# Optimization experiments

Hardware: AMD Instinct MI355X
Metric: run time of the kernel (lower is better)

Reference implementation:

```python
import jax, jax.numpy as jnp
import numpy as np

B, D_IN, UNITS = 4096, 1024, 1024


def setup_inputs() -> dict:
    key = jax.random.key(0)
    ks = jax.random.split(key, 8)
    scale = 1.0 / np.sqrt(D_IN + UNITS)
    return {
        "inputs": jax.random.normal(ks[0], (B, D_IN), jnp.float32),
        "hidden_state": jax.random.normal(ks[1], (B, UNITS), jnp.float32),
        "cell_state": jax.random.normal(ks[2], (B, UNITS), jnp.float32),
        "W_f": jax.random.normal(ks[3], (D_IN + UNITS, UNITS), jnp.float32) * scale,
        "b_f": jnp.ones((UNITS,), jnp.float32),  # forget gate bias initialized to ones
        "W_i": jax.random.normal(ks[4], (D_IN + UNITS, UNITS), jnp.float32) * scale,
        "b_i": jnp.zeros((UNITS,), jnp.float32),
        "W_c": jax.random.normal(ks[5], (D_IN + UNITS, UNITS), jnp.float32) * scale,
        "b_c": jnp.zeros((UNITS,), jnp.float32),
        "W_o": jax.random.normal(ks[6], (D_IN + UNITS, UNITS), jnp.float32) * scale,
        "b_o": jnp.zeros((UNITS,), jnp.float32),
    }


def reference(inputs, hidden_state, cell_state, W_f, b_f, W_i, b_i, W_c, b_c, W_o, b_o):
    # concat (hidden, inputs) along feature axis -> [B, UNITS + D_IN]
    x = jnp.concatenate((hidden_state, inputs), axis=1)
    # fuse the 4 gate projections into one GEMM: [B, 4*UNITS]
    W = jnp.concatenate((W_f, W_i, W_c, W_o), axis=1)
    b = jnp.concatenate((b_f, b_i, b_c, b_o), axis=0)
    gates = x @ W + b
    f, i, c, o = jnp.split(gates, 4, axis=1)
    forget_gate = jax.nn.sigmoid(f)
    input_gate = jax.nn.sigmoid(i)
    state_candidates = jnp.tanh(c)
    output_gate = jax.nn.sigmoid(o)
    new_cell = forget_gate * cell_state + input_gate * state_candidates
    new_hidden = output_gate * jnp.tanh(new_cell)
    return (new_hidden, new_cell)
```

## Files before the change

### kernel.cpp

```cpp
#include <hip/hip_runtime.h>

#define MDIM 4096
#define KDIM 2048
#define UDIM 1024
#define CMOFF (MDIM * UDIM)
#define NK 64
#define THREADS 512

typedef __bf16 bfrag __attribute__((ext_vector_type(8)));
typedef float f32x16 __attribute__((ext_vector_type(16)));

#define GLDS(gsrc, ldst)                                                                  \
  __builtin_amdgcn_global_load_lds((const __attribute__((address_space(1))) void*)(gsrc), \
                                   (__attribute__((address_space(3))) void*)(ldst), 16, 0, 0)

__device__ __forceinline__ unsigned short f2bf(float x) {
  unsigned int u = __float_as_uint(x);
  unsigned int r = (u + 0x7fffu + ((u >> 16) & 1u)) >> 16;
  return (unsigned short)r;
}

__device__ __forceinline__ float fast_sigmoid(float x) { return 1.f / (1.f + __expf(-x)); }

__device__ __forceinline__ float fast_tanh(float x) {
  float ax = fabsf(x);
  float e = __expf(-2.f * ax);
  float r = (1.f - e) / (1.f + e);
  return copysignf(r, x);
}

__global__ void pack_x(const float* __restrict__ hidden, const float* __restrict__ inputs,
                       unsigned short* __restrict__ A) {
  int t = blockIdx.x * blockDim.x + threadIdx.x;
  int e = t * 4;
  int m = e >> 11;
  int c = e & 2047;
  const float* src = (c < 1024) ? (hidden + m * 1024 + c) : (inputs + m * 1024 + (c - 1024));
  float4 v = *(const float4*)src;
  ushort4 o;
  o.x = f2bf(v.x);
  o.y = f2bf(v.y);
  o.z = f2bf(v.z);
  o.w = f2bf(v.w);
  *(ushort4*)(A + e) = o;
}

__global__ void pack_w(const float* __restrict__ Wf, const float* __restrict__ Wi,
                       const float* __restrict__ Wc, const float* __restrict__ Wo,
                       unsigned short* __restrict__ Wt) {
  __shared__ float tile[32][33];
  const int k0 = blockIdx.x * 32;
  const int u0 = blockIdx.y * 32;
  const int g = blockIdx.z;
  const float* W = (g == 0) ? Wf : (g == 1) ? Wi : (g == 2) ? Wc : Wo;
  const int t = threadIdx.x;
  {
    int kk = t >> 3, uu = (t & 7) * 4;
    float4 v = *(const float4*)(W + (k0 + kk) * UDIM + u0 + uu);
    tile[kk][uu + 0] = v.x;
    tile[kk][uu + 1] = v.y;
    tile[kk][uu + 2] = v.z;
    tile[kk][uu + 3] = v.w;
  }
  __syncthreads();
  {
    int ur = t >> 3, k4 = (t & 7) * 4;
    ushort4 o;
    o.x = f2bf(tile[k4 + 0][ur]);
    o.y = f2bf(tile[k4 + 1][ur]);
    o.z = f2bf(tile[k4 + 2][ur]);
    o.w = f2bf(tile[k4 + 3][ur]);
    *(ushort4*)(Wt + (size_t)(g * UDIM + u0 + ur) * KDIM + k0 + k4) = o;
  }
}

__global__ __launch_bounds__(THREADS, 2) void lstm_gemm(
    const unsigned short* __restrict__ A, const unsigned short* __restrict__ Wt,
    const float* __restrict__ bf_, const float* __restrict__ bi_,
    const float* __restrict__ bc_, const float* __restrict__ bo_,
    const float* __restrict__ cell, float* __restrict__ out) {
  extern __shared__ __bf16 lds[];

  const int tid = threadIdx.x;
  const int lane = tid & 63;
  const int wid = tid >> 6;
  const int wr = wid >> 1;
  const int wc = wid & 1;
  const int cl = lane & 31;
  const int hb = lane >> 5;

  const int wg = blockIdx.x;
  const int swz = (wg & 7) * 32 + (wg >> 3);
  const int m0 = (swz >> 4) * 256;
  const int bn = swz & 15;

  const int G0 = tid, G1 = THREADS + tid;
  const int ar0 = G0 >> 2, ar1 = G1 >> 2;
  const unsigned short* aS0 =
      A + (size_t)(m0 + ar0) * KDIM + (((G0 & 3) ^ ((ar0 >> 1) & 3)) * 8);
  const unsigned short* aS1 =
      A + (size_t)(m0 + ar1) * KDIM + (((G1 & 3) ^ ((ar1 >> 1) & 3)) * 8);
  const int nr0 = G0 >> 2, nr1 = G1 >> 2;
  const int u_0 = bn * 64 + ((nr0 >> 7) << 5) + (nr0 & 31);
  const int u_1 = bn * 64 + ((nr1 >> 7) << 5) + (nr1 & 31);
  const int g_0 = (nr0 >> 5) & 3;
  const int g_1 = (nr1 >> 5) & 3;
  const unsigned short* bS0 =
      Wt + (size_t)(g_0 * UDIM + u_0) * KDIM + (((G0 & 3) ^ ((nr0 >> 1) & 3)) * 8);
  const unsigned short* bS1 =
      Wt + (size_t)(g_1 * UDIM + u_1) * KDIM + (((G1 & 3) ^ ((nr1 >> 1) & 3)) * 8);

  int aoff2[2][2];
#pragma unroll
  for (int mf = 0; mf < 2; ++mf)
#pragma unroll
    for (int kk = 0; kk < 2; ++kk) {
      const int R = wr * 64 + mf * 32 + cl;
      aoff2[mf][kk] = R * 32 + (((kk * 2 + hb) ^ ((R >> 1) & 3)) * 8);
    }
  int boff2[4][2];
#pragma unroll
  for (int nf = 0; nf < 4; ++nf)
#pragma unroll
    for (int kk = 0; kk < 2; ++kk) {
      const int n = wc * 128 + nf * 32 + cl;
      boff2[nf][kk] = 8192 + n * 32 + (((kk * 2 + hb) ^ ((n >> 1) & 3)) * 8);
    }

  f32x16 acc[2][4];
#pragma unroll
  for (int mf = 0; mf < 2; ++mf)
#pragma unroll
    for (int nf = 0; nf < 4; ++nf)
#pragma unroll
      for (int j = 0; j < 16; ++j) acc[mf][nf][j] = 0.f;

#define STAGE_A(T, SR)                        \
  do {                                        \
    __bf16* dst_ = lds + (SR) * 16384;        \
    GLDS(aS0 + (T) * 32, dst_ + G0 * 8);      \
    GLDS(aS1 + (T) * 32, dst_ + G1 * 8);      \
  } while (0)
#define STAGE_B(T, SR)                        \
  do {                                        \
    __bf16* dst_ = lds + (SR) * 16384 + 8192; \
    GLDS(bS0 + (T) * 32, dst_ + G0 * 8);      \
    GLDS(bS1 + (T) * 32, dst_ + G1 * 8);      \
  } while (0)

  STAGE_A(0, 0);
  STAGE_B(0, 0);
  STAGE_A(1, 1);
  STAGE_B(1, 1);
  STAGE_A(2, 2);
  STAGE_B(2, 2);
  asm volatile("s_waitcnt vmcnt(8)" ::: "memory");
  __builtin_amdgcn_s_barrier();

#define TILE_BODY(T, R, SR, DO_STAGE, WAITCODE)                                          \
  do {                                                                                   \
    __bf16* ldsr_ = lds + (R) * 16384;                                                   \
    bfrag Af[2][2], Bf[4][2];                                                            \
    _Pragma("unroll") for (int mf = 0; mf < 2; ++mf) Af[mf][0] =                         \
        *(const bfrag*)(ldsr_ + aoff2[mf][0]);                                           \
    _Pragma("unroll") for (int nf = 0; nf < 4; ++nf) Bf[nf][0] =                         \
        *(const bfrag*)(ldsr_ + boff2[nf][0]);                                           \
    _Pragma("unroll") for (int mf = 0; mf < 2; ++mf) Af[mf][1] =                         \
        *(const bfrag*)(ldsr_ + aoff2[mf][1]);                                           \
    _Pragma("unroll") for (int nf = 0; nf < 4; ++nf) Bf[nf][1] =                         \
        *(const bfrag*)(ldsr_ + boff2[nf][1]);                                           \
    if (DO_STAGE) {                                                                      \
      STAGE_A((T) + 3, SR);                                                              \
      STAGE_B((T) + 3, SR);                                                              \
    }                                                                                    \
    __builtin_amdgcn_s_barrier();                                                        \
    __builtin_amdgcn_s_setprio(1);                                                       \
    _Pragma("unroll") for (int kk = 0; kk < 2; ++kk)                                     \
        _Pragma("unroll") for (int mf = 0; mf < 2; ++mf)                                 \
            _Pragma("unroll") for (int nf = 0; nf < 4; ++nf) acc[mf][nf] =               \
                __builtin_amdgcn_mfma_f32_32x32x16_bf16(Af[mf][kk], Bf[nf][kk],          \
                                                        acc[mf][nf], 0, 0, 0);           \
    __builtin_amdgcn_s_setprio(0);                                                       \
    WAITCODE;                                                                            \
    __builtin_amdgcn_s_barrier();                                                        \
  } while (0)

#define VM8 asm volatile("s_waitcnt vmcnt(8)" ::: "memory")
#define VM4 asm volatile("s_waitcnt vmcnt(4)" ::: "memory")
#define VM0 asm volatile("s_waitcnt vmcnt(0)" ::: "memory")

  for (int t = 0; t < NK - 4; t += 4) {
    TILE_BODY(t + 0, 0, 3, 1, VM8);
    TILE_BODY(t + 1, 1, 0, 1, VM8);
    TILE_BODY(t + 2, 2, 1, 1, VM8);
    TILE_BODY(t + 3, 3, 2, 1, VM8);
  }
  TILE_BODY(NK - 4, 0, 3, 1, VM8);
  TILE_BODY(NK - 3, 1, 0, 0, VM4);
  TILE_BODY(NK - 2, 2, 0, 0, VM0);
  TILE_BODY(NK - 1, 3, 0, 0, );

  const int u = bn * 64 + wc * 32 + cl;
  const float fb = bf_[u], ib = bi_[u], cb = bc_[u], ob = bo_[u];
  const int rbase = m0 + wr * 64 + 4 * hb;
#pragma unroll
  for (int mf = 0; mf < 2; ++mf) {
#pragma unroll
    for (int r = 0; r < 16; ++r) {
      const int m = rbase + mf * 32 + (r & 3) + 8 * (r >> 2);
      float pf = acc[mf][0][r] + fb;
      float pi = acc[mf][1][r] + ib;
      float pc = acc[mf][2][r] + cb;
      float po = acc[mf][3][r] + ob;
      float fg = fast_sigmoid(pf);
      float ig = fast_sigmoid(pi);
      float cc = fast_tanh(pc);
      float og = fast_sigmoid(po);
      float cold = cell[(size_t)m * UDIM + u];
      float cnew = fg * cold + ig * cc;
      out[(size_t)m * UDIM + u] = og * fast_tanh(cnew);
      out[CMOFF + (size_t)m * UDIM + u] = cnew;
    }
  }
}

extern "C" void kernel_launch(void* const* d_in, const int* in_sizes, int n_in,
                              void* d_out, int out_size, void* d_ws, size_t ws_size,
                              hipStream_t stream) {
  const float* inputs = (const float*)d_in[0];
  const float* hidden = (const float*)d_in[1];
  const float* cell = (const float*)d_in[2];
  const float* Wf = (const float*)d_in[3];
  const float* bf = (const float*)d_in[4];
  const float* Wi = (const float*)d_in[5];
  const float* bi = (const float*)d_in[6];
  const float* Wc = (const float*)d_in[7];
  const float* bc = (const float*)d_in[8];
  const float* Wo = (const float*)d_in[9];
  const float* bo = (const float*)d_in[10];
  float* out = (float*)d_out;

  unsigned short* Abf = (unsigned short*)d_ws;
  unsigned short* Wt = Abf + (size_t)MDIM * KDIM;

  pack_x<<<(MDIM * KDIM / 4) / 256, 256, 0, stream>>>(hidden, inputs, Abf);
  pack_w<<<dim3(KDIM / 32, UDIM / 32, 4), 256, 0, stream>>>(Wf, Wi, Wc, Wo, Wt);
  lstm_gemm<<<dim3(256), dim3(THREADS), 131072, stream>>>(Abf, Wt, bf, bi, bc, bo, cell, out);
}
```

Baseline: 99.18 us.

## Pre-pack operands into tile-contiguous blocks and switch GEMM to double-buffered K=64 steps

The pack kernels now write A and the transposed weights in a tile-blocked layout, so each 256x64 (A) or 256x64 (B) K-slab is one contiguous 32 KB chunk. The GEMM loads each slab with fully contiguous global_load_lds transfers and reads MFMA fragments with simple strided offsets, with no XOR swizzle. The old 4-deep ring of K=32 tiles becomes a 2-deep ring of K=64 tiles with a full vmcnt(0) wait per step. The aim is cheaper address math, fewer barriers and more coalesced packing. The trade-off is shallower prefetch, and the unswizzled LDS reads may cause bank conflicts.

```diff
diff --git a/kernel.cpp b/kernel.cpp
--- a/kernel.cpp
+++ b/kernel.cpp
@@ -4,7 +4,6 @@
 #define KDIM 2048
 #define UDIM 1024
 #define CMOFF (MDIM * UDIM)
-#define NK 64
 #define THREADS 512
 
 typedef __bf16 bfrag __attribute__((ext_vector_type(8)));
@@ -29,53 +28,68 @@
   return copysignf(r, x);
 }
 
+
 __global__ void pack_x(const float* __restrict__ hidden, const float* __restrict__ inputs,
-                       unsigned short* __restrict__ A) {
-  int t = blockIdx.x * blockDim.x + threadIdx.x;
-  int e = t * 4;
-  int m = e >> 11;
-  int c = e & 2047;
-  const float* src = (c < 1024) ? (hidden + m * 1024 + c) : (inputs + m * 1024 + (c - 1024));
-  float4 v = *(const float4*)src;
-  ushort4 o;
-  o.x = f2bf(v.x);
-  o.y = f2bf(v.y);
-  o.z = f2bf(v.z);
-  o.w = f2bf(v.w);
-  *(ushort4*)(A + e) = o;
+                       unsigned short* __restrict__ Apk) {
+  __shared__ uint4 t4[2048];
+  const int P = blockIdx.x;
+  const int S = blockIdx.y;
+  const int tid = threadIdx.x;
+  const size_t m = (size_t)P * 256 + tid;
+  const float* src = (S < 16) ? (hidden + m * 1024 + S * 64) : (inputs + m * 1024 + (S - 16) * 64);
+  const float4* s4 = (const float4*)src;
+#pragma unroll
+  for (int j = 0; j < 8; ++j) {
+    float4 v0 = s4[2 * j], v1 = s4[2 * j + 1];
+    uint4 g;
+    g.x = (unsigned)f2bf(v0.x) | ((unsigned)f2bf(v0.y) << 16);
+    g.y = (unsigned)f2bf(v0.z) | ((unsigned)f2bf(v0.w) << 16);
+    g.z = (unsigned)f2bf(v1.x) | ((unsigned)f2bf(v1.y) << 16);
+    g.w = (unsigned)f2bf(v1.z) | ((unsigned)f2bf(v1.w) << 16);
+    t4[j * 256 + tid] = g;
+  }
+  __syncthreads();
+  uint4* dst = (uint4*)(Apk + ((size_t)P * 32 + S) * 16384);
+#pragma unroll
+  for (int c = 0; c < 8; ++c) dst[c * 256 + tid] = t4[c * 256 + tid];
 }
 
 __global__ void pack_w(const float* __restrict__ Wf, const float* __restrict__ Wi,
                        const float* __restrict__ Wc, const float* __restrict__ Wo,
-                       unsigned short* __restrict__ Wt) {
-  __shared__ float tile[32][33];
-  const int k0 = blockIdx.x * 32;
-  const int u0 = blockIdx.y * 32;
-  const int g = blockIdx.z;
-  const float* W = (g == 0) ? Wf : (g == 1) ? Wi : (g == 2) ? Wc : Wo;
-  const int t = threadIdx.x;
-  {
-    int kk = t >> 3, uu = (t & 7) * 4;
-    float4 v = *(const float4*)(W + (k0 + kk) * UDIM + u0 + uu);
-    tile[kk][uu + 0] = v.x;
-    tile[kk][uu + 1] = v.y;
-    tile[kk][uu + 2] = v.z;
-    tile[kk][uu + 3] = v.w;
+                       unsigned short* __restrict__ Bpk) {
+  __shared__ unsigned short t1[4][64][64];
+  const int bn = blockIdx.x;
+  const int S = blockIdx.y;
+  const int tid = threadIdx.x;
+  const int q = tid >> 6, kk = tid & 63;
+  const float* W = (q == 0) ? Wf : (q == 1) ? Wi : (q == 2) ? Wc : Wo;
+  const float* src = W + (size_t)(S * 64 + kk) * UDIM + bn * 64;
+#pragma unroll
+  for (int i = 0; i < 16; ++i) {
+    float4 v = ((const float4*)src)[i];
+    t1[q][kk][i * 4 + 0] = f2bf(v.x);
+    t1[q][kk][i * 4 + 1] = f2bf(v.y);
+    t1[q][kk][i * 4 + 2] = f2bf(v.z);
+    t1[q][kk][i * 4 + 3] = f2bf(v.w);
   }
   __syncthreads();
-  {
-    int ur = t >> 3, k4 = (t & 7) * 4;
-    ushort4 o;
-    o.x = f2bf(tile[k4 + 0][ur]);
-    o.y = f2bf(tile[k4 + 1][ur]);
-    o.z = f2bf(tile[k4 + 2][ur]);
-    o.w = f2bf(tile[k4 + 3][ur]);
-    *(ushort4*)(Wt + (size_t)(g * UDIM + u0 + ur) * KDIM + k0 + k4) = o;
+  const int qp = (tid >> 5) & 3;
+  const int ul = ((tid >> 7) << 5) + (tid & 31);
+  uint4* dst = (uint4*)(Bpk + ((size_t)bn * 32 + S) * 16384);
+#pragma unroll
+  for (int c = 0; c < 8; ++c) {
+    const unsigned short* p = &t1[qp][c * 8][ul];
+    uint4 g;
+    g.x = (unsigned)p[0] | ((unsigned)p[64] << 16);
+    g.y = (unsigned)p[128] | ((unsigned)p[192] << 16);
+    g.z = (unsigned)p[256] | ((unsigned)p[320] << 16);
+    g.w = (unsigned)p[384] | ((unsigned)p[448] << 16);
+    dst[c * 256 + tid] = g;
   }
 }
 
 __global__ __launch_bounds__(THREADS, 2) void lstm_gemm(
-    const unsigned short* __restrict__ A, const unsigned short* __restrict__ Wt,
+    const unsigned short* __restrict__ Apk, const unsigned short* __restrict__ Bpk,
     const float* __restrict__ bf_, const float* __restrict__ bi_,
     const float* __restrict__ bc_, const float* __restrict__ bo_,
     const float* __restrict__ cell, float* __restrict__ out) {
@@ -91,114 +105,70 @@
 
   const int wg = blockIdx.x;
   const int swz = (wg & 7) * 32 + (wg >> 3);
-  const int m0 = (swz >> 4) * 256;
+  const int P = swz >> 4;
+  const int m0 = P * 256;
   const int bn = swz & 15;
 
-  const int G0 = tid, G1 = THREADS + tid;
-  const int ar0 = G0 >> 2, ar1 = G1 >> 2;
-  const unsigned short* aS0 =
-      A + (size_t)(m0 + ar0) * KDIM + (((G0 & 3) ^ ((ar0 >> 1) & 3)) * 8);
-  const unsigned short* aS1 =
-      A + (size_t)(m0 + ar1) * KDIM + (((G1 & 3) ^ ((ar1 >> 1) & 3)) * 8);
-  const int nr0 = G0 >> 2, nr1 = G1 >> 2;
-  const int u_0 = bn * 64 + ((nr0 >> 7) << 5) + (nr0 & 31);
-  const int u_1 = bn * 64 + ((nr1 >> 7) << 5) + (nr1 & 31);
-  const int g_0 = (nr0 >> 5) & 3;
-  const int g_1 = (nr1 >> 5) & 3;
-  const unsigned short* bS0 =
-      Wt + (size_t)(g_0 * UDIM + u_0) * KDIM + (((G0 & 3) ^ ((nr0 >> 1) & 3)) * 8);
-  const unsigned short* bS1 =
-      Wt + (size_t)(g_1 * UDIM + u_1) * KDIM + (((G1 & 3) ^ ((nr1 >> 1) & 3)) * 8);
-
-  int aoff2[2][2];
+  const unsigned short* aP = Apk + (size_t)P * 524288 + (size_t)tid * 8;
+  const unsigned short* bP = Bpk + (size_t)bn * 524288 + (size_t)tid * 8;
+
+  f32x16 acc[2][4];
 #pragma unroll
   for (int mf = 0; mf < 2; ++mf)
 #pragma unroll
-    for (int kk = 0; kk < 2; ++kk) {
-      const int R = wr * 64 + mf * 32 + cl;
-      aoff2[mf][kk] = R * 32 + (((kk * 2 + hb) ^ ((R >> 1) & 3)) * 8);
-    }
-  int boff2[4][2];
-#pragma unroll
-  for (int nf = 0; nf < 4; ++nf)
-#pragma unroll
-    for (int kk = 0; kk < 2; ++kk) {
-      const int n = wc * 128 + nf * 32 + cl;
-      boff2[nf][kk] = 8192 + n * 32 + (((kk * 2 + hb) ^ ((n >> 1) & 3)) * 8);
-    }
-
-  f32x16 acc[2][4];
-#pragma unroll
-  for (int mf = 0; mf < 2; ++mf)
-#pragma unroll
     for (int nf = 0; nf < 4; ++nf)
 #pragma unroll
       for (int j = 0; j < 16; ++j) acc[mf][nf][j] = 0.f;
 
-#define STAGE_A(T, SR)                        \
-  do {                                        \
-    __bf16* dst_ = lds + (SR) * 16384;        \
-    GLDS(aS0 + (T) * 32, dst_ + G0 * 8);      \
-    GLDS(aS1 + (T) * 32, dst_ + G1 * 8);      \
+  const int aBase = hb * 2048 + (wr * 64 + cl) * 8;
+  const int bBase = 16384 + hb * 2048 + (wc * 128 + cl) * 8;
+
+#define STAGE(RING)                                                               \
+  do {                                                                            \
+    _Pragma("unroll") for (int c = 0; c < 4; ++c)                                 \
+        GLDS(aP + c * 4096, lds + (RING) * 32768 + c * 4096 + tid * 8);           \
+    _Pragma("unroll") for (int c = 0; c < 4; ++c)                                 \
+        GLDS(bP + c * 4096, lds + (RING) * 32768 + 16384 + c * 4096 + tid * 8);   \
+    aP += 16384;                                                                  \
+    bP += 16384;                                                                  \
   } while (0)
-#define STAGE_B(T, SR)                        \
-  do {                                        \
-    __bf16* dst_ = lds + (SR) * 16384 + 8192; \
-    GLDS(bS0 + (T) * 32, dst_ + G0 * 8);      \
-    GLDS(bS1 + (T) * 32, dst_ + G1 * 8);      \
+
+#define STEP_BODY(RING, DO_STAGE)                                                     \
+  do {                                                                                \
+    asm volatile("s_waitcnt vmcnt(0)" ::: "memory");                                  \
+    __builtin_amdgcn_s_barrier();                                                     \
+    __builtin_amdgcn_sched_barrier(0);                                                \
+    if (DO_STAGE) STAGE((RING) ^ 1);                                                  \
+    const __bf16* apl = lds + (RING) * 32768 + aBase;                                 \
+    const __bf16* bpl = lds + (RING) * 32768 + bBase;                                 \
+    _Pragma("unroll") for (int ks = 0; ks < 4; ++ks) {                                \
+      bfrag a0 = *(const bfrag*)(apl + ks * 4096);                                    \
+      bfrag a1 = *(const bfrag*)(apl + ks * 4096 + 256);                              \
+      bfrag b0 = *(const bfrag*)(bpl + ks * 4096);                                    \
+      bfrag b1 = *(const bfrag*)(bpl + ks * 4096 + 256);                              \
+      bfrag b2 = *(const bfrag*)(bpl + ks * 4096 + 512);                              \
+      bfrag b3 = *(const bfrag*)(bpl + ks * 4096 + 768);                              \
+      __builtin_amdgcn_s_setprio(1);                                                  \
+      acc[0][0] = __builtin_amdgcn_mfma_f32_32x32x16_bf16(a0, b0, acc[0][0], 0, 0, 0);\
+      acc[0][1] = __builtin_amdgcn_mfma_f32_32x32x16_bf16(a0, b1, acc[0][1], 0, 0, 0);\
+      acc[0][2] = __builtin_amdgcn_mfma_f32_32x32x16_bf16(a0, b2, acc[0][2], 0, 0, 0);\
+      acc[0][3] = __builtin_amdgcn_mfma_f32_32x32x16_bf16(a0, b3, acc[0][3], 0, 0, 0);\
+      acc[1][0] = __builtin_amdgcn_mfma_f32_32x32x16_bf16(a1, b0, acc[1][0], 0, 0, 0);\
+      acc[1][1] = __builtin_amdgcn_mfma_f32_32x32x16_bf16(a1, b1, acc[1][1], 0, 0, 0);\
+      acc[1][2] = __builtin_amdgcn_mfma_f32_32x32x16_bf16(a1, b2, acc[1][2], 0, 0, 0);\
+      acc[1][3] = __builtin_amdgcn_mfma_f32_32x32x16_bf16(a1, b3, acc[1][3], 0, 0, 0);\
+      __builtin_amdgcn_s_setprio(0);                                                  \
+    }                                                                                 \
   } while (0)
 
-  STAGE_A(0, 0);
-  STAGE_B(0, 0);
-  STAGE_A(1, 1);
-  STAGE_B(1, 1);
-  STAGE_A(2, 2);
-  STAGE_B(2, 2);
-  asm volatile("s_waitcnt vmcnt(8)" ::: "memory");
-  __builtin_amdgcn_s_barrier();
-
-#define TILE_BODY(T, R, SR, DO_STAGE, WAITCODE)                                          \
-  do {                                                                                   \
-    __bf16* ldsr_ = lds + (R) * 16384;                                                   \
-    bfrag Af[2][2], Bf[4][2];                                                            \
-    _Pragma("unroll") for (int mf = 0; mf < 2; ++mf) Af[mf][0] =                         \
-        *(const bfrag*)(ldsr_ + aoff2[mf][0]);                                           \
-    _Pragma("unroll") for (int nf = 0; nf < 4; ++nf) Bf[nf][0] =                         \
-        *(const bfrag*)(ldsr_ + boff2[nf][0]);                                           \
-    _Pragma("unroll") for (int mf = 0; mf < 2; ++mf) Af[mf][1] =                         \
-        *(const bfrag*)(ldsr_ + aoff2[mf][1]);                                           \
-    _Pragma("unroll") for (int nf = 0; nf < 4; ++nf) Bf[nf][1] =                         \
-        *(const bfrag*)(ldsr_ + boff2[nf][1]);                                           \
-    if (DO_STAGE) {                                                                      \
-      STAGE_A((T) + 3, SR);                                                              \
-      STAGE_B((T) + 3, SR);                                                              \
-    }                                                                                    \
-    __builtin_amdgcn_s_barrier();                                                        \
-    __builtin_amdgcn_s_setprio(1);                                                       \
-    _Pragma("unroll") for (int kk = 0; kk < 2; ++kk)                                     \
-        _Pragma("unroll") for (int mf = 0; mf < 2; ++mf)                                 \
-            _Pragma("unroll") for (int nf = 0; nf < 4; ++nf) acc[mf][nf] =               \
-                __builtin_amdgcn_mfma_f32_32x32x16_bf16(Af[mf][kk], Bf[nf][kk],          \
-                                                        acc[mf][nf], 0, 0, 0);           \
-    __builtin_amdgcn_s_setprio(0);                                                       \
-    WAITCODE;                                                                            \
-    __builtin_amdgcn_s_barrier();                                                        \
-  } while (0)
-
-#define VM8 asm volatile("s_waitcnt vmcnt(8)" ::: "memory")
-#define VM4 asm volatile("s_waitcnt vmcnt(4)" ::: "memory")
-#define VM0 asm volatile("s_waitcnt vmcnt(0)" ::: "memory")
-
-  for (int t = 0; t < NK - 4; t += 4) {
-    TILE_BODY(t + 0, 0, 3, 1, VM8);
-    TILE_BODY(t + 1, 1, 0, 1, VM8);
-    TILE_BODY(t + 2, 2, 1, 1, VM8);
-    TILE_BODY(t + 3, 3, 2, 1, VM8);
-  }
-  TILE_BODY(NK - 4, 0, 3, 1, VM8);
-  TILE_BODY(NK - 3, 1, 0, 0, VM4);
-  TILE_BODY(NK - 2, 2, 0, 0, VM0);
-  TILE_BODY(NK - 1, 3, 0, 0, );
+  STAGE(0);
+
+  for (int it = 0; it < 15; ++it) {
+    STEP_BODY(0, 1);
+    STEP_BODY(1, 1);
+  }
+  STEP_BODY(0, 1);
+  STEP_BODY(1, 0);
 
   const int u = bn * 64 + wc * 32 + cl;
   const float fb = bf_[u], ib = bi_[u], cb = bc_[u], ob = bo_[u];
@@ -240,10 +210,10 @@
   const float* bo = (const float*)d_in[10];
   float* out = (float*)d_out;
 
-  unsigned short* Abf = (unsigned short*)d_ws;
-  unsigned short* Wt = Abf + (size_t)MDIM * KDIM;
-
-  pack_x<<<(MDIM * KDIM / 4) / 256, 256, 0, stream>>>(hidden, inputs, Abf);
-  pack_w<<<dim3(KDIM / 32, UDIM / 32, 4), 256, 0, stream>>>(Wf, Wi, Wc, Wo, Wt);
-  lstm_gemm<<<dim3(256), dim3(THREADS), 131072, stream>>>(Abf, Wt, bf, bi, bc, bo, cell, out);
-}
+  unsigned short* Apk = (unsigned short*)d_ws;
+  unsigned short* Bpk = Apk + (size_t)MDIM * KDIM;
+
+  pack_x<<<dim3(16, 32), 256, 0, stream>>>(hidden, inputs, Apk);
+  pack_w<<<dim3(16, 32), 256, 0, stream>>>(Wf, Wi, Wc, Wo, Bpk);
+  lstm_gemm<<<dim3(256), dim3(THREADS), 131072, stream>>>(Apk, Bpk, bf, bi, bc, bo, cell, out);
+}
```

Result: faster. 92.34 us (-6.9%).
